# Kernel optimization log

Measured on AMD Instinct MI355X. Metric: run time of the kernel, lower is better.

## Reference

```python
import jax, jax.numpy as jnp
import numpy as np

N_PAPER = 50000
N_AUTHOR = 50000
E = 400000
N_FEAT = 256
N_HID = 256
N_CLASS = 128
TEMP = 1.0  # cfg.temparature


def setup_inputs() -> dict:
    key = jax.random.key(0)
    ks = jax.random.split(key, 40)
    def lin_init(k, shape, fan_in):
        s = 1.0 / np.sqrt(fan_in)
        return jax.random.uniform(k, shape, jnp.float32, -s, s)
    inp = {}
    inp['x_paper'] = jax.random.normal(ks[0], (N_PAPER, N_FEAT), jnp.float32)
    # xavier-uniform embedding for featureless node type 'author'
    xs = np.sqrt(6.0 / (N_AUTHOR + N_FEAT))
    inp['emb_author'] = jax.random.uniform(ks[1], (N_AUTHOR, N_FEAT), jnp.float32, -xs, xs)
    i = 2
    for l, fin in [(0, N_FEAT), (1, N_HID)]:
        for nt in ['paper', 'author']:
            inp[f'l{l}_root_{nt}_W'] = lin_init(ks[i], (fin, N_HID), fin); i += 1
            inp[f'l{l}_root_{nt}_b'] = lin_init(ks[i], (N_HID,), fin); i += 1
        for et in ['writes', 'rev', 'cites']:
            inp[f'l{l}_rel_{et}_W'] = lin_init(ks[i], (fin, N_HID), fin); i += 1
    inp['out_W'] = lin_init(ks[i], (N_HID, N_CLASS), N_HID); i += 1
    inp['out_b'] = lin_init(ks[i], (N_CLASS,), N_HID); i += 1
    inp['writes_src'] = jax.random.randint(ks[i], (E,), 0, N_AUTHOR); i += 1
    inp['writes_dst'] = jax.random.randint(ks[i], (E,), 0, N_PAPER); i += 1
    inp['rev_src'] = jax.random.randint(ks[i], (E,), 0, N_PAPER); i += 1
    inp['rev_dst'] = jax.random.randint(ks[i], (E,), 0, N_AUTHOR); i += 1
    inp['cites_src'] = jax.random.randint(ks[i], (E,), 0, N_PAPER); i += 1
    inp['cites_dst'] = jax.random.randint(ks[i], (E,), 0, N_PAPER); i += 1
    return inp


def _mean_agg(x_src, src, dst, n_dst):
    # sparse adj_t.matmul(x, reduce='mean'): segment-sum of gathered rows / in-degree (0 for isolated)
    msg = jax.ops.segment_sum(x_src[src], dst, num_segments=n_dst)  # [n_dst, d]
    deg = jax.ops.segment_sum(jnp.ones(src.shape[0], x_src.dtype), dst, num_segments=n_dst)
    return jnp.where(deg[:, None] > 0, msg / jnp.maximum(deg, 1.0)[:, None], 0.0)


def reference(x_paper, emb_author,
              l0_root_paper_W, l0_root_paper_b, l0_root_author_W, l0_root_author_b,
              l0_rel_writes_W, l0_rel_rev_W, l0_rel_cites_W,
              l1_root_paper_W, l1_root_paper_b, l1_root_author_W, l1_root_author_b,
              l1_rel_writes_W, l1_rel_rev_W, l1_rel_cites_W,
              out_W, out_b,
              writes_src, writes_dst, rev_src, rev_dst, cites_src, cites_dst):
    nnodes = {'paper': x_paper.shape[0], 'author': emb_author.shape[0]}
    # (src_type, dst_type, src_idx, dst_idx, rel_slot)
    edges = [('author', 'paper', writes_src, writes_dst, 0),
             ('paper', 'author', rev_src, rev_dst, 1),
             ('paper', 'paper', cites_src, cites_dst, 2)]
    layers = [
        {'root': {'paper': (l0_root_paper_W, l0_root_paper_b), 'author': (l0_root_author_W, l0_root_author_b)},
         'rel': [l0_rel_writes_W, l0_rel_rev_W, l0_rel_cites_W]},
        {'root': {'paper': (l1_root_paper_W, l1_root_paper_b), 'author': (l1_root_author_W, l1_root_author_b)},
         'rel': [l1_rel_writes_W, l1_rel_rev_W, l1_rel_cites_W]},
    ]
    xd = {'paper': x_paper, 'author': emb_author}
    xd_ = dict(xd)  # twin path starts from same features
    hs, hs_ = [], []
    for p in layers:
        out = {k: xd[k] @ p['root'][k][0] + p['root'][k][1] for k in xd}
        out_ = {k: xd_[k] @ p['root'][k][0] + p['root'][k][1] for k in xd_}
        for s, d, src, dst, slot in edges:
            W = p['rel'][slot]
            out[d] = out[d] + _mean_agg(xd[s], src, dst, nnodes[d]) @ W
            out_[d] = out_[d] + xd_[d] @ W  # twin path: no propagation, same rel transform
        xd = {k: jax.nn.relu(v) for k, v in out.items()}   # dropout is identity (eval)
        xd_ = {k: jax.nn.relu(v) for k, v in out_.items()}
        hs.append(xd['paper'])
        hs_.append(xd_['paper'])
    # Summarize: per-node dot-product attention over layer representations
    H = jnp.stack(hs)    # [L, N, d]
    H_ = jnp.stack(hs_)  # [L, N, d]
    alpha = jax.nn.softmax(jnp.sum(H * H_, axis=-1) / TEMP, axis=0)  # [L, N]
    h = jnp.sum(alpha[..., None] * H, axis=0)  # [N, d]
    logits = h @ out_W + out_b
    return (logits, alpha)
```

## Files before the change

kernel.cpp:

```cpp
#include <hip/hip_runtime.h>
#include <hip/hip_bf16.h>

#define NFEAT 256

typedef __attribute__((ext_vector_type(8))) short bf16x8;
typedef __attribute__((ext_vector_type(4))) float f32x4;
typedef __attribute__((ext_vector_type(8))) unsigned short us8;

__device__ __forceinline__ void f2hilo(float x, unsigned short& h, unsigned short& l) {
    __hip_bfloat16 hb = __float2bfloat16(x);
    float hf = __bfloat162float(hb);
    __hip_bfloat16 lb = __float2bfloat16(x - hf);
    h = *reinterpret_cast<unsigned short*>(&hb);
    l = *reinterpret_cast<unsigned short*>(&lb);
}

__global__ __launch_bounds__(256) void cvt8_kernel(
    const float* w0, const float* w1, const float* w2, const float* w3,
    const float* w4, const float* w5, const float* w6, const float* w7,
    unsigned short* base)
{
    int wi = blockIdx.y;
    const float* W = (wi==0)?w0:(wi==1)?w1:(wi==2)?w2:(wi==3)?w3:
                     (wi==4)?w4:(wi==5)?w5:(wi==6)?w6:w7;
    int idx = blockIdx.x * 256 + threadIdx.x;
    int k = idx >> 8, c = idx & 255;
    unsigned short h, l;
    f2hilo(W[idx], h, l);
    size_t dst = ((size_t)((c >> 7) * 8 + (k >> 5)) * 128 + (c & 127)) * 32 + (k & 31);
    unsigned short* Th = base + (size_t)wi * 131072;
    Th[dst] = h;
    Th[65536 + dst] = l;
}

__global__ __launch_bounds__(256) void cvtfold_kernel(
    const float* a0, const float* a1, const float* a2,
    const float* b0, const float* b1, const float* b2,
    unsigned short* base)
{
    int wi = blockIdx.y;
    int idx = blockIdx.x * 256 + threadIdx.x;
    float v = wi ? (b0[idx] + b1[idx] + b2[idx]) : (a0[idx] + a1[idx] + a2[idx]);
    int k = idx >> 8, c = idx & 255;
    unsigned short h, l;
    f2hilo(v, h, l);
    size_t dst = ((size_t)((c >> 7) * 8 + (k >> 5)) * 128 + (c & 127)) * 32 + (k & 31);
    unsigned short* Th = base + (size_t)(8 + wi) * 131072;
    Th[dst] = h;
    Th[65536 + dst] = l;
}

__global__ __launch_bounds__(256) void cvtrect_kernel(const float* W, unsigned short* base) {
    int idx = blockIdx.x * 256 + threadIdx.x;
    if (idx >= 256 * 128) return;
    int k = idx >> 7, c = idx & 127;
    unsigned short h, l;
    f2hilo(W[idx], h, l);
    size_t dst = ((size_t)(k >> 5) * 128 + c) * 32 + (k & 31);
    unsigned short* Th = base + (size_t)10 * 131072;
    Th[dst] = h;
    Th[65536 + dst] = l;
}

__global__ __launch_bounds__(256) void deg_int_kernel(const int* __restrict__ dst,
                                                      int* __restrict__ deg, int nE) {
    int e = blockIdx.x * 256 + threadIdx.x;
    if (e < nE) atomicAdd(&deg[dst[e]], 1);
}

__global__ __launch_bounds__(256) void scan_p1(const int* __restrict__ deg, int n,
                                               int* __restrict__ off, int* __restrict__ bsum) {
    __shared__ int tmp[256];
    int tid = threadIdx.x;
    int i = blockIdx.x * 256 + tid;
    tmp[tid] = (i < n) ? deg[i] : 0;
    __syncthreads();
    #pragma unroll
    for (int ofs = 1; ofs < 256; ofs <<= 1) {
        int t = (tid >= ofs) ? tmp[tid - ofs] : 0;
        __syncthreads();
        tmp[tid] += t;
        __syncthreads();
    }
    if (i < n) off[i + 1] = tmp[tid];
    if (tid == 255) bsum[blockIdx.x] = tmp[255];
}

__global__ __launch_bounds__(256) void scan_p2(int* __restrict__ bA, int nA,
                                               int* __restrict__ bB, int nB,
                                               int* __restrict__ bC, int nC) {
    int* bs; int nb;
    if (blockIdx.x == 0) { bs = bA; nb = nA; }
    else if (blockIdx.x == 1) { bs = bB; nb = nB; }
    else { bs = bC; nb = nC; }
// ... 48 lines not shown
        acc.x += v.x; acc.y += v.y; acc.z += v.z; acc.w += v.w;
    }
    int cnt = end - start;
    float inv = (cnt > 0) ? 1.0f / (float)cnt : 0.0f;
    float4 d;
    if (mode_add) {
        d = ((float4*)(D + (size_t)r * NFEAT))[lane];
        d.x += acc.x * inv; d.y += acc.y * inv;
        d.z += acc.z * inv; d.w += acc.w * inv;
    } else {
        d.x = acc.x * inv; d.y = acc.y * inv;
        d.z = acc.z * inv; d.w = acc.w * inv;
    }
    if (do_relu) {
        d.x = fmaxf(d.x, 0.f); d.y = fmaxf(d.y, 0.f);
        d.z = fmaxf(d.z, 0.f); d.w = fmaxf(d.w, 0.f);
    }
    ((float4*)(D + (size_t)r * NFEAT))[lane] = d;
}

__global__ __launch_bounds__(256) void alpha_kernel(const float* __restrict__ s0,
                                                    const float* __restrict__ s1,
                                                    float* __restrict__ alpha, int M) {
    int n = blockIdx.x * 256 + threadIdx.x;
    if (n >= M) return;
    float v0 = s0[n], v1 = s1[n];
    float m = fmaxf(v0, v1);
    float e0 = expf(v0 - m), e1 = expf(v1 - m);
    float inv = 1.0f / (e0 + e1);
    alpha[n]     = e0 * inv;
    alpha[M + n] = e1 * inv;
}


struct Seg3 {
    const float *A0, *A1, *A2;
    const unsigned short *Wh0, *Wl0, *Wh1, *Wl1, *Wh2, *Wl2;
};

__global__ __launch_bounds__(256, 3) void gemm_ms(
    Seg3 sp, int nseg, const float* __restrict__ bias, int do_relu,
    float* __restrict__ C, int M, int N)
{
    __shared__ unsigned short Ah[128 * 32];
    __shared__ unsigned short Al[128 * 32];

    int tid = threadIdx.x;
    int lane = tid & 63;
    int w = tid >> 6;
    int wr = w >> 1, wc = w & 1;
    int row0 = blockIdx.x * 128, cb = blockIdx.y, col0 = cb * 128;
    int fr = lane & 15;
    int fg = lane >> 4;

    int sr = tid & 127;
    int sh = tid >> 7;
    int grow = row0 + sr; if (grow >= M) grow = M - 1;
    int wbase = (((sr >> 4) * 64) + (sh * 2) * 16 + (sr & 15)) * 8;

    f32x4 acc[4][4];
    #pragma unroll
    for (int m = 0; m < 4; ++m)
        #pragma unroll
        for (int n = 0; n < 4; ++n)
            acc[m][n] = (f32x4)(0.f);

    for (int s = 0; s < 3; ++s) {
        if (s >= nseg) break;
        const float* Xrow = ((s == 0) ? sp.A0 : (s == 1) ? sp.A1 : sp.A2) + (size_t)grow * NFEAT;
        const unsigned short* Wh = (s == 0) ? sp.Wh0 : (s == 1) ? sp.Wh1 : sp.Wh2;
        const unsigned short* Wl = (s == 0) ? sp.Wl0 : (s == 1) ? sp.Wl1 : sp.Wl2;

        for (int k0 = 0; k0 < NFEAT; k0 += 32) {
            unsigned short hh[16], ll[16];
            #pragma unroll
            for (int q = 0; q < 4; ++q) {
                float4 v = *(const float4*)(Xrow + k0 + sh * 16 + q * 4);
                f2hilo(v.x, hh[q*4+0], ll[q*4+0]);
                f2hilo(v.y, hh[q*4+1], ll[q*4+1]);
                f2hilo(v.z, hh[q*4+2], ll[q*4+2]);
                f2hilo(v.w, hh[q*4+3], ll[q*4+3]);
            }
            __syncthreads();
            *(us8*)&Ah[wbase]       = *(us8*)&hh[0];
            *(us8*)&Ah[wbase + 128] = *(us8*)&hh[8];
            *(us8*)&Al[wbase]       = *(us8*)&ll[0];
            *(us8*)&Al[wbase + 128] = *(us8*)&ll[8];
            __syncthreads();

            const unsigned short* WhB = Wh + (size_t)(cb * 8 + (k0 >> 5)) * 4096;
            const unsigned short* WlB = Wl + (size_t)(cb * 8 + (k0 >> 5)) * 4096;

            bf16x8 ahf[4], alf[4], bhf[4], blf[4];
            #pragma unroll
            for (int m = 0; m < 4; ++m) {
                int g = ((wr * 4 + m) * 64 + lane) * 8;
                ahf[m] = *(const bf16x8*)&Ah[g];
                alf[m] = *(const bf16x8*)&Al[g];
            }
            #pragma unroll
            for (int n = 0; n < 4; ++n) {
                int o = (wc * 64 + n * 16 + fr) * 32 + fg * 8;
                bhf[n] = *(const bf16x8*)(WhB + o);
                blf[n] = *(const bf16x8*)(WlB + o);
            }
            #pragma unroll
            for (int m = 0; m < 4; ++m)
                #pragma unroll
                for (int n = 0; n < 4; ++n) {
                    acc[m][n] = __builtin_amdgcn_mfma_f32_16x16x32_bf16(ahf[m], bhf[n], acc[m][n], 0, 0, 0);
                    acc[m][n] = __builtin_amdgcn_mfma_f32_16x16x32_bf16(alf[m], bhf[n], acc[m][n], 0, 0, 0);
                    acc[m][n] = __builtin_amdgcn_mfma_f32_16x16x32_bf16(ahf[m], blf[n], acc[m][n], 0, 0, 0);
                }
        }
    }

    #pragma unroll
    for (int n = 0; n < 4; ++n) {
        int c = col0 + wc * 64 + n * 16 + fr;
        float bv = bias ? bias[c] : 0.f;
        #pragma unroll
        for (int m = 0; m < 4; ++m) {
            int rbase = row0 + wr * 64 + m * 16 + fg * 4;
            #pragma unroll
            for (int i = 0; i < 4; ++i) {
                int r = rbase + i;
                if (r < M) {
                    float v = acc[m][n][i] + bv;
                    if (do_relu) v = fmaxf(v, 0.f);
                    C[(size_t)r * N + c] = v;
                }
            }
        }
    }
}

__global__ __launch_bounds__(256, 3) void gemm_rowdot_mfma(
    const float* __restrict__ X,
    const unsigned short* __restrict__ Wh, const unsigned short* __restrict__ Wl,
    const float* __restrict__ bias,
    const float* __restrict__ P, const float* __restrict__ Q,
    float* __restrict__ s0g, float* __restrict__ s1g, int M)
{
    __shared__ unsigned short Ah[128 * 32];
    __shared__ unsigned short Al[128 * 32];
    __shared__ float srow[128];
    __shared__ float s0buf[256];

    int tid = threadIdx.x;
    int lane = tid & 63;
    int w = tid >> 6;
    int wr = w >> 1, wc = w & 1;
    int row0 = blockIdx.x * 128;
    int fr = lane & 15;
    int fg = lane >> 4;

    int sr = tid & 127;
    int sh = tid >> 7;
    int grow = row0 + sr; if (grow >= M) grow = M - 1;
    int wbase = (((sr >> 4) * 64) + (sh * 2) * 16 + (sr & 15)) * 8;

    if (tid < 128) srow[tid] = 0.f;
    float s0part = 0.f;

    const float* Xrow = X + (size_t)grow * NFEAT;
    const float* Qrow = Q + (size_t)grow * NFEAT;

    float rp[4][4];
    #pragma unroll
    for (int m = 0; m < 4; ++m)
        #pragma unroll
        for (int i = 0; i < 4; ++i) rp[m][i] = 0.f;

    for (int ct = 0; ct < 2; ++ct) {
        f32x4 acc[4][4];
        #pragma unroll
        for (int m = 0; m < 4; ++m)
            #pragma unroll
            for (int n = 0; n < 4; ++n)
                acc[m][n] = (f32x4)(0.f);

        for (int k0 = 0; k0 < NFEAT; k0 += 32) {
            unsigned short hh[16], ll[16];
            #pragma unroll
            for (int q = 0; q < 4; ++q) {
                float4 v = *(const float4*)(Xrow + k0 + sh * 16 + q * 4);
                if (ct == 0) {
                    float4 qv = *(const float4*)(Qrow + k0 + sh * 16 + q * 4);
                    s0part += v.x * qv.x + v.y * qv.y + v.z * qv.z + v.w * qv.w;
                }
                f2hilo(v.x, hh[q*4+0], ll[q*4+0]);
                f2hilo(v.y, hh[q*4+1], ll[q*4+1]);
                f2hilo(v.z, hh[q*4+2], ll[q*4+2]);
                f2hilo(v.w, hh[q*4+3], ll[q*4+3]);
            }
            __syncthreads();
            *(us8*)&Ah[wbase]       = *(us8*)&hh[0];
            *(us8*)&Ah[wbase + 128] = *(us8*)&hh[8];
            *(us8*)&Al[wbase]       = *(us8*)&ll[0];
            *(us8*)&Al[wbase + 128] = *(us8*)&ll[8];
            __syncthreads();

            const unsigned short* WhB = Wh + (size_t)(ct * 8 + (k0 >> 5)) * 4096;
            const unsigned short* WlB = Wl + (size_t)(ct * 8 + (k0 >> 5)) * 4096;

            bf16x8 ahf[4], alf[4], bhf[4], blf[4];
            #pragma unroll
            for (int m = 0; m < 4; ++m) {
                int g = ((wr * 4 + m) * 64 + lane) * 8;
                ahf[m] = *(const bf16x8*)&Ah[g];
                alf[m] = *(const bf16x8*)&Al[g];
            }
            #pragma unroll
            for (int n = 0; n < 4; ++n) {
                int o = (wc * 64 + n * 16 + fr) * 32 + fg * 8;
                bhf[n] = *(const bf16x8*)(WhB + o);
                blf[n] = *(const bf16x8*)(WlB + o);
            }
            #pragma unroll
            for (int m = 0; m < 4; ++m)
                #pragma unroll
                for (int n = 0; n < 4; ++n) {
                    acc[m][n] = __builtin_amdgcn_mfma_f32_16x16x32_bf16(ahf[m], bhf[n], acc[m][n], 0, 0, 0);
                    acc[m][n] = __builtin_amdgcn_mfma_f32_16x16x32_bf16(alf[m], bhf[n], acc[m][n], 0, 0, 0);
                    acc[m][n] = __builtin_amdgcn_mfma_f32_16x16x32_bf16(ahf[m], blf[n], acc[m][n], 0, 0, 0);
                }
        }

        int col0 = ct * 128;
        #pragma unroll
        for (int n = 0; n < 4; ++n) {
            int c = col0 + wc * 64 + n * 16 + fr;
            float bv = bias[c];
            #pragma unroll
            for (int m = 0; m < 4; ++m) {
                #pragma unroll
                for (int i = 0; i < 4; ++i) {
                    int r = row0 + wr * 64 + m * 16 + fg * 4 + i;
                    if (r < M) {
                        float v = fmaxf(acc[m][n][i] + bv, 0.f);
                        rp[m][i] += v * P[(size_t)r * NFEAT + c];
                    }
                }
            }
        }
    }

    s0buf[tid] = s0part;

    #pragma unroll
    for (int o = 1; o < 16; o <<= 1) {
        #pragma unroll
        for (int m = 0; m < 4; ++m)
            #pragma unroll
            for (int i = 0; i < 4; ++i)
                rp[m][i] += __shfl_xor(rp[m][i], o);
    }
    if ((lane & 15) == 0) {
        #pragma unroll
        for (int m = 0; m < 4; ++m)
            #pragma unroll
            for (int i = 0; i < 4; ++i)
                atomicAdd(&srow[wr * 64 + m * 16 + fg * 4 + i], rp[m][i]);
    }
    __syncthreads();
    if (tid < 128 && row0 + tid < M) {
        s1g[row0 + tid] = srow[tid];
        s0g[row0 + tid] = s0buf[tid] + s0buf[tid + 128];
    }
}

__global__ __launch_bounds__(256, 3) void gemm_head(
    const float* __restrict__ P1, const float* __restrict__ P2,
    const float* __restrict__ alpha,
    const unsigned short* __restrict__ Wh, const unsigned short* __restrict__ Wl,
    const float* __restrict__ bias,
    float* __restrict__ C, int M, int N)
{
    __shared__ unsigned short Ah[128 * 32];
    __shared__ unsigned short Al[128 * 32];

    int tid = threadIdx.x;
    int lane = tid & 63;
    int w = tid >> 6;
    int wr = w >> 1, wc = w & 1;
    int row0 = blockIdx.x * 128;
    int fr = lane & 15;
    int fg = lane >> 4;

    int sr = tid & 127;
    int sh = tid >> 7;
    int grow = row0 + sr; if (grow >= M) grow = M - 1;
    int wbase = (((sr >> 4) * 64) + (sh * 2) * 16 + (sr & 15)) * 8;

    const float* P1row = P1 + (size_t)grow * NFEAT;
    const float* P2row = P2 + (size_t)grow * NFEAT;
    float a0 = alpha[grow], a1 = alpha[M + grow];

    f32x4 acc[4][4];
    #pragma unroll
    for (int m = 0; m < 4; ++m)
        #pragma unroll
        for (int n = 0; n < 4; ++n)
            acc[m][n] = (f32x4)(0.f);

    for (int k0 = 0; k0 < NFEAT; k0 += 32) {
        unsigned short hh[16], ll[16];
        #pragma unroll
        for (int q = 0; q < 4; ++q) {
            float4 u = *(const float4*)(P1row + k0 + sh * 16 + q * 4);
            float4 v = *(const float4*)(P2row + k0 + sh * 16 + q * 4);
            float4 x = make_float4(a0*u.x + a1*v.x, a0*u.y + a1*v.y,
                                   a0*u.z + a1*v.z, a0*u.w + a1*v.w);
            f2hilo(x.x, hh[q*4+0], ll[q*4+0]);
            f2hilo(x.y, hh[q*4+1], ll[q*4+1]);
            f2hilo(x.z, hh[q*4+2], ll[q*4+2]);
            f2hilo(x.w, hh[q*4+3], ll[q*4+3]);
        }
        __syncthreads();
        *(us8*)&Ah[wbase]       = *(us8*)&hh[0];
        *(us8*)&Ah[wbase + 128] = *(us8*)&hh[8];
        *(us8*)&Al[wbase]       = *(us8*)&ll[0];
        *(us8*)&Al[wbase + 128] = *(us8*)&ll[8];
        __syncthreads();

        const unsigned short* WhB = Wh + (size_t)(k0 >> 5) * 4096;
        const unsigned short* WlB = Wl + (size_t)(k0 >> 5) * 4096;

        bf16x8 ahf[4], alf[4], bhf[4], blf[4];
        #pragma unroll
        for (int m = 0; m < 4; ++m) {
            int g = ((wr * 4 + m) * 64 + lane) * 8;
            ahf[m] = *(const bf16x8*)&Ah[g];
            alf[m] = *(const bf16x8*)&Al[g];
        }
        #pragma unroll
        for (int n = 0; n < 4; ++n) {
            int o = (wc * 64 + n * 16 + fr) * 32 + fg * 8;
            bhf[n] = *(const bf16x8*)(WhB + o);
            blf[n] = *(const bf16x8*)(WlB + o);
        }
        #pragma unroll
        for (int m = 0; m < 4; ++m)
            #pragma unroll
            for (int n = 0; n < 4; ++n) {
                acc[m][n] = __builtin_amdgcn_mfma_f32_16x16x32_bf16(ahf[m], bhf[n], acc[m][n], 0, 0, 0);
                acc[m][n] = __builtin_amdgcn_mfma_f32_16x16x32_bf16(alf[m], bhf[n], acc[m][n], 0, 0, 0);
                acc[m][n] = __builtin_amdgcn_mfma_f32_16x16x32_bf16(ahf[m], blf[n], acc[m][n], 0, 0, 0);
            }
    }

    #pragma unroll
    for (int n = 0; n < 4; ++n) {
        int c = wc * 64 + n * 16 + fr;
        if (c >= N) continue;
        float bv = bias[c];
        #pragma unroll
        for (int m = 0; m < 4; ++m) {
            int rbase = row0 + wr * 64 + m * 16 + fg * 4;
            #pragma unroll
            for (int i = 0; i < 4; ++i) {
                int r = rbase + i;
                if (r < M) C[(size_t)r * N + c] = acc[m][n][i] + bv;
            }
        }
    }
}

extern "C" void kernel_launch(void* const* d_in, const int* in_sizes, int n_in,
                              void* d_out, int out_size, void* d_ws, size_t ws_size,
                              hipStream_t stream)
{
    const float* x_paper    = (const float*)d_in[0];
// ... 44 lines not shown
    int* bsW  = offC + NP + 1;
    int* bsR  = bsW + 256;
    int* bsC  = bsR + 256;
    int* listW = bsC + 256;
    int* listR = listW + nEw;
    int* listC = listR + nEr;

    float* out   = (float*)d_out;
    float* alpha = out + (size_t)NP * NC;

    hipMemsetAsync(degW, 0, (size_t)2 * (NP + NA + NP) * sizeof(int), stream);
    deg_int_kernel<<<(nEw + 255) / 256, 256, 0, stream>>>(w_dst, degW, nEw);
    deg_int_kernel<<<(nEr + 255) / 256, 256, 0, stream>>>(r_dst, degR, nEr);
    deg_int_kernel<<<(nEc + 255) / 256, 256, 0, stream>>>(c_dst, degC, nEc);

    int nbP = (NP + 255) / 256, nbA = (NA + 255) / 256;
    scan_p1<<<nbP, 256, 0, stream>>>(degW, NP, offW, bsW);
    scan_p1<<<nbA, 256, 0, stream>>>(degR, NA, offR, bsR);
    scan_p1<<<nbP, 256, 0, stream>>>(degC, NP, offC, bsC);
    scan_p2<<<3, 256, 0, stream>>>(bsW, nbP, bsR, nbA, bsC, nbP);
    scan_p3<<<nbP, 256, 0, stream>>>(NP, offW, bsW);
    scan_p3<<<nbA, 256, 0, stream>>>(NA, offR, bsR);
    scan_p3<<<nbP, 256, 0, stream>>>(NP, offC, bsC);

    fill_csr_kernel<<<(nEw + 255) / 256, 256, 0, stream>>>(w_src, w_dst, nEw, offW, curW, listW);
    fill_csr_kernel<<<(nEr + 255) / 256, 256, 0, stream>>>(r_src, r_dst, nEr, offR, curR, listR);
    fill_csr_kernel<<<(nEc + 255) / 256, 256, 0, stream>>>(c_src, c_dst, nEc, offC, curC, listC);

    cvt8_kernel<<<dim3(256, 8), 256, 0, stream>>>(W0rp, W0w, W0c, W0ra, W0rev, W1rp, W1w, W1c, Wt);
    cvtfold_kernel<<<dim3(256, 2), 256, 0, stream>>>(W0rp, W0w, W0c, W1rp, W1w, W1c, Wt);
    cvtrect_kernel<<<128, 256, 0, stream>>>(outW, Wt);

    dim3 blk(256);
    dim3 gP((NP + 127) / 128, 2);
    dim3 gA((NA + 127) / 128, 2);
    dim3 g1((NP + 127) / 128);
    int nodeP = (NP + 3) / 4, nodeA = (NA + 3) / 4;

    agg_csr_kernel<<<nodeP, blk, 0, stream>>>(emb_author, offW, listW, Z0, 0, 0, NP);
    agg_csr_kernel<<<nodeP, blk, 0, stream>>>(x_paper,    offC, listC, Z1, 0, 0, NP);
    {
        Seg3 sp = {x_paper, Z0, Z1, WT_HI(0), WT_LO(0), WT_HI(1), WT_LO(1), WT_HI(2), WT_LO(2)};
        gemm_ms<<<gP, blk, 0, stream>>>(sp, 3, b0rp, 1, Z2, NP, NFEAT);
    }
    agg_csr_kernel<<<nodeA, blk, 0, stream>>>(x_paper, offR, listR, Z0, 0, 0, NA);
    {
        Seg3 sp = {emb_author, Z0, nullptr, WT_HI(3), WT_LO(3), WT_HI(4), WT_LO(4), nullptr, nullptr};
        gemm_ms<<<gA, blk, 0, stream>>>(sp, 2, b0ra, 1, Z1, NA, NFEAT);
    }

    agg_csr_kernel<<<nodeP, blk, 0, stream>>>(Z1, offW, listW, Z0, 0, 0, NP);
    {
        Seg3 sp = {Z2, Z0, nullptr, WT_HI(5), WT_LO(5), WT_HI(6), WT_LO(6), nullptr, nullptr};
        gemm_ms<<<gP, blk, 0, stream>>>(sp, 2, b1rp, 0, Z1, NP, NFEAT);
    }
    {
        Seg3 sp = {Z2, nullptr, nullptr, WT_HI(7), WT_LO(7), nullptr, nullptr, nullptr, nullptr};
        gemm_ms<<<gP, blk, 0, stream>>>(sp, 1, nullptr, 0, Z0, NP, NFEAT);
    }
    agg_csr_kernel<<<nodeP, blk, 0, stream>>>(Z0, offC, listC, Z1, 1, 1, NP);

    {
        Seg3 sp = {x_paper, nullptr, nullptr, WT_HI(8), WT_LO(8), nullptr, nullptr, nullptr, nullptr};
        gemm_ms<<<gP, blk, 0, stream>>>(sp, 1, b0rp, 1, Z0, NP, NFEAT);
    }
    gemm_rowdot_mfma<<<g1, blk, 0, stream>>>(Z0, WT_HI(9), WT_LO(9), b1rp, Z1, Z2, s0, s1, NP);

    alpha_kernel<<<(NP + 255) / 256, blk, 0, stream>>>(s0, s1, alpha, NP);
// ... 3 lines not shown
```

Measured before the change: 948.1 us.

## Prefetch next K-tile into registers and stage weights through LDS in GEMMs

The three MFMA GEMM kernels now issue the global loads for the next K-slice (activations and bf16 hi/lo weights) right after the LDS barrier, so they overlap with the current tile's MFMAs. Weights are cooperatively loaded into new shared-memory B tiles instead of being read directly from global memory by each wave. The row-dot kernel flattens its two column passes into one 16-step pipelined loop, and gemm_ms interleaves its two column blocks along grid x so neighbouring blocks share A rows. LDS per block doubles and the occupancy hint drops from 3 to 2 blocks per CU, which may limit latency hiding.

Result: no change. 949.5 us (+0.1%).

```diff
diff --git a/kernel.cpp b/kernel.cpp
--- a/kernel.cpp
+++ b/kernel.cpp
@@ -13,6 +13,25 @@
     __hip_bfloat16 lb = __float2bfloat16(x - hf);
     h = *reinterpret_cast<unsigned short*>(&hb);
     l = *reinterpret_cast<unsigned short*>(&lb);
+}
+
+__device__ __forceinline__ void load_a16(const float* __restrict__ p, float* af) {
+    float4 u0 = ((const float4*)p)[0];
+    float4 u1 = ((const float4*)p)[1];
+    float4 u2 = ((const float4*)p)[2];
+    float4 u3 = ((const float4*)p)[3];
+    af[0]=u0.x; af[1]=u0.y; af[2]=u0.z; af[3]=u0.w;
+    af[4]=u1.x; af[5]=u1.y; af[6]=u1.z; af[7]=u1.w;
+    af[8]=u2.x; af[9]=u2.y; af[10]=u2.z; af[11]=u2.w;
+    af[12]=u3.x; af[13]=u3.y; af[14]=u3.z; af[15]=u3.w;
+}
+
+__device__ __forceinline__ void load_b(const unsigned short* __restrict__ ph,
+                                       const unsigned short* __restrict__ pl, us8* bb) {
+    bb[0] = *(const us8*)ph;
+    bb[1] = *(const us8*)(ph + 8);
+    bb[2] = *(const us8*)pl;
+    bb[3] = *(const us8*)(pl + 8);
 }
 
 __global__ __launch_bounds__(256) void cvt8_kernel(
@@ -174,24 +193,26 @@
     alpha[M + n] = e1 * inv;
 }
 
-
 struct Seg3 {
     const float *A0, *A1, *A2;
     const unsigned short *Wh0, *Wl0, *Wh1, *Wl1, *Wh2, *Wl2;
 };
 
-__global__ __launch_bounds__(256, 3) void gemm_ms(
+__global__ __launch_bounds__(256, 2) void gemm_ms(
     Seg3 sp, int nseg, const float* __restrict__ bias, int do_relu,
     float* __restrict__ C, int M, int N)
 {
     __shared__ unsigned short Ah[128 * 32];
     __shared__ unsigned short Al[128 * 32];
+    __shared__ unsigned short Bh[128 * 32];
+    __shared__ unsigned short Bl[128 * 32];
 
     int tid = threadIdx.x;
     int lane = tid & 63;
     int w = tid >> 6;
     int wr = w >> 1, wc = w & 1;
-    int row0 = blockIdx.x * 128, cb = blockIdx.y, col0 = cb * 128;
+    int rb = blockIdx.x >> 1, cb = blockIdx.x & 1;
+    int row0 = rb * 128, col0 = cb * 128;
     int fr = lane & 15;
     int fg = lane >> 4;
 
@@ -200,6 +221,10 @@
     int grow = row0 + sr; if (grow >= M) grow = M - 1;
     int wbase = (((sr >> 4) * 64) + (sh * 2) * 16 + (sr & 15)) * 8;
 
+    int bc = tid >> 1;
+    int bk = (tid & 1) * 16;
+    int bbase = (((bc >> 4) * 64) + (tid & 1) * 2 * 16 + (bc & 15)) * 8;
+
     f32x4 acc[4][4];
     #pragma unroll
     for (int m = 0; m < 4; ++m)
@@ -207,54 +232,59 @@
         for (int n = 0; n < 4; ++n)
             acc[m][n] = (f32x4)(0.f);
 
-    for (int s = 0; s < 3; ++s) {
-        if (s >= nseg) break;
-        const float* Xrow = ((s == 0) ? sp.A0 : (s == 1) ? sp.A1 : sp.A2) + (size_t)grow * NFEAT;
-        const unsigned short* Wh = (s == 0) ? sp.Wh0 : (s == 1) ? sp.Wh1 : sp.Wh2;
-        const unsigned short* Wl = (s == 0) ? sp.Wl0 : (s == 1) ? sp.Wl1 : sp.Wl2;
-
-        for (int k0 = 0; k0 < NFEAT; k0 += 32) {
-            unsigned short hh[16], ll[16];
-            #pragma unroll
-            for (int q = 0; q < 4; ++q) {
-                float4 v = *(const float4*)(Xrow + k0 + sh * 16 + q * 4);
-                f2hilo(v.x, hh[q*4+0], ll[q*4+0]);
-                f2hilo(v.y, hh[q*4+1], ll[q*4+1]);
-                f2hilo(v.z, hh[q*4+2], ll[q*4+2]);
-                f2hilo(v.w, hh[q*4+3], ll[q*4+3]);
+    int niters = nseg * 8;
+    float af[16];
+    us8 bb[4];
+    load_a16(sp.A0 + (size_t)grow * NFEAT + sh * 16, af);
+    load_b(sp.Wh0 + (size_t)(cb * 8) * 4096 + bc * 32 + bk,
+           sp.Wl0 + (size_t)(cb * 8) * 4096 + bc * 32 + bk, bb);
+
+    for (int it = 0; it < niters; ++it) {
+        unsigned short hh[16], ll[16];
+        #pragma unroll
+        for (int j = 0; j < 16; ++j) f2hilo(af[j], hh[j], ll[j]);
+        __syncthreads();
+        *(us8*)&Ah[wbase]       = *(us8*)&hh[0];
+        *(us8*)&Ah[wbase + 128] = *(us8*)&hh[8];
+        *(us8*)&Al[wbase]       = *(us8*)&ll[0];
+        *(us8*)&Al[wbase + 128] = *(us8*)&ll[8];
+        *(us8*)&Bh[bbase]       = bb[0];
+        *(us8*)&Bh[bbase + 128] = bb[1];
+        *(us8*)&Bl[bbase]       = bb[2];
+        *(us8*)&Bl[bbase + 128] = bb[3];
+        __syncthreads();
+
+        if (it + 1 < niters) {
+            int s = (it + 1) >> 3, kq = (it + 1) & 7;
+            const float* A = (s == 0) ? sp.A0 : (s == 1) ? sp.A1 : sp.A2;
+            const unsigned short* Wh = (s == 0) ? sp.Wh0 : (s == 1) ? sp.Wh1 : sp.Wh2;
+            const unsigned short* Wl = (s == 0) ? sp.Wl0 : (s == 1) ? sp.Wl1 : sp.Wl2;
+            load_a16(A + (size_t)grow * NFEAT + kq * 32 + sh * 16, af);
+            load_b(Wh + (size_t)(cb * 8 + kq) * 4096 + bc * 32 + bk,
+                   Wl + (size_t)(cb * 8 + kq) * 4096 + bc * 32 + bk, bb);
+        }
+
+        bf16x8 ahf[4], alf[4], bhf[4], blf[4];
+        #pragma unroll
+        for (int m = 0; m < 4; ++m) {
+            int g = ((wr * 4 + m) * 64 + lane) * 8;
+            ahf[m] = *(const bf16x8*)&Ah[g];
+            alf[m] = *(const bf16x8*)&Al[g];
+        }
+        #pragma unroll
+        for (int n = 0; n < 4; ++n) {
+            int g = ((wc * 4 + n) * 64 + lane) * 8;
+            bhf[n] = *(const bf16x8*)&Bh[g];
+            blf[n] = *(const bf16x8*)&Bl[g];
+        }
+        #pragma unroll
+        for (int m = 0; m < 4; ++m)
+            #pragma unroll
+            for (int n = 0; n < 4; ++n) {
+                acc[m][n] = __builtin_amdgcn_mfma_f32_16x16x32_bf16(ahf[m], bhf[n], acc[m][n], 0, 0, 0);
+                acc[m][n] = __builtin_amdgcn_mfma_f32_16x16x32_bf16(alf[m], bhf[n], acc[m][n], 0, 0, 0);
+                acc[m][n] = __builtin_amdgcn_mfma_f32_16x16x32_bf16(ahf[m], blf[n], acc[m][n], 0, 0, 0);
             }
-            __syncthreads();
-            *(us8*)&Ah[wbase]       = *(us8*)&hh[0];
-            *(us8*)&Ah[wbase + 128] = *(us8*)&hh[8];
-            *(us8*)&Al[wbase]       = *(us8*)&ll[0];
-            *(us8*)&Al[wbase + 128] = *(us8*)&ll[8];
-            __syncthreads();
-
-            const unsigned short* WhB = Wh + (size_t)(cb * 8 + (k0 >> 5)) * 4096;
-            const unsigned short* WlB = Wl + (size_t)(cb * 8 + (k0 >> 5)) * 4096;
-
-            bf16x8 ahf[4], alf[4], bhf[4], blf[4];
-            #pragma unroll
-            for (int m = 0; m < 4; ++m) {
-                int g = ((wr * 4 + m) * 64 + lane) * 8;
-                ahf[m] = *(const bf16x8*)&Ah[g];
-                alf[m] = *(const bf16x8*)&Al[g];
-            }
-            #pragma unroll
-            for (int n = 0; n < 4; ++n) {
-                int o = (wc * 64 + n * 16 + fr) * 32 + fg * 8;
-                bhf[n] = *(const bf16x8*)(WhB + o);
-                blf[n] = *(const bf16x8*)(WlB + o);
-            }
-            #pragma unroll
-            for (int m = 0; m < 4; ++m)
-                #pragma unroll
-                for (int n = 0; n < 4; ++n) {
-                    acc[m][n] = __builtin_amdgcn_mfma_f32_16x16x32_bf16(ahf[m], bhf[n], acc[m][n], 0, 0, 0);
-                    acc[m][n] = __builtin_amdgcn_mfma_f32_16x16x32_bf16(alf[m], bhf[n], acc[m][n], 0, 0, 0);
-                    acc[m][n] = __builtin_amdgcn_mfma_f32_16x16x32_bf16(ahf[m], blf[n], acc[m][n], 0, 0, 0);
-                }
-        }
     }
 
     #pragma unroll
@@ -277,7 +307,7 @@
     }
 }
 
-__global__ __launch_bounds__(256, 3) void gemm_rowdot_mfma(
+__global__ __launch_bounds__(256, 2) void gemm_rowdot_mfma(
     const float* __restrict__ X,
     const unsigned short* __restrict__ Wh, const unsigned short* __restrict__ Wl,
     const float* __restrict__ bias,
@@ -286,6 +316,8 @@
 {
     __shared__ unsigned short Ah[128 * 32];
     __shared__ unsigned short Al[128 * 32];
+    __shared__ unsigned short Bh[128 * 32];
+    __shared__ unsigned short Bl[128 * 32];
     __shared__ float srow[128];
     __shared__ float s0buf[256];
 
@@ -301,12 +333,15 @@
     int sh = tid >> 7;
     int grow = row0 + sr; if (grow >= M) grow = M - 1;
     int wbase = (((sr >> 4) * 64) + (sh * 2) * 16 + (sr & 15)) * 8;
+    int bc = tid >> 1;
+    int bk = (tid & 1) * 16;
+    int bbase = (((bc >> 4) * 64) + (tid & 1) * 2 * 16 + (bc & 15)) * 8;
 
     if (tid < 128) srow[tid] = 0.f;
     float s0part = 0.f;
 
-    const float* Xrow = X + (size_t)grow * NFEAT;
-    const float* Qrow = Q + (size_t)grow * NFEAT;
+    const float* Xrow = X + (size_t)grow * NFEAT + sh * 16;
+    const float* Qrow = Q + (size_t)grow * NFEAT + sh * 16;
 
     float rp[4][4];
     #pragma unroll
@@ -314,77 +349,91 @@
         #pragma unroll
         for (int i = 0; i < 4; ++i) rp[m][i] = 0.f;
 
-    for (int ct = 0; ct < 2; ++ct) {
-        f32x4 acc[4][4];
+    f32x4 acc[4][4];
+    #pragma unroll
+    for (int m = 0; m < 4; ++m)
+        #pragma unroll
+        for (int n = 0; n < 4; ++n)
+            acc[m][n] = (f32x4)(0.f);
+
+    float af[16], qf[16];
+    us8 bb[4];
+    load_a16(Xrow, af);
+    load_a16(Qrow, qf);
+    load_b(Wh + bc * 32 + bk, Wl + bc * 32 + bk, bb);
+
+    for (int it = 0; it < 16; ++it) {
+        if (it < 8) {
+            #pragma unroll
+            for (int j = 0; j < 16; ++j) s0part += af[j] * qf[j];
+        }
+        unsigned short hh[16], ll[16];
+        #pragma unroll
+        for (int j = 0; j < 16; ++j) f2hilo(af[j], hh[j], ll[j]);
+        __syncthreads();
+        *(us8*)&Ah[wbase]       = *(us8*)&hh[0];
+        *(us8*)&Ah[wbase + 128] = *(us8*)&hh[8];
+        *(us8*)&Al[wbase]       = *(us8*)&ll[0];
+        *(us8*)&Al[wbase + 128] = *(us8*)&ll[8];
+        *(us8*)&Bh[bbase]       = bb[0];
+        *(us8*)&Bh[bbase + 128] = bb[1];
+        *(us8*)&Bl[bbase]       = bb[2];
+        *(us8*)&Bl[bbase + 128] = bb[3];
+        __syncthreads();
+
+        if (it + 1 < 16) {
+            int kq = (it + 1) & 7;
+            load_a16(Xrow + kq * 32, af);
+            if (it + 1 < 8) load_a16(Qrow + kq * 32, qf);
+            load_b(Wh + (size_t)(it + 1) * 4096 + bc * 32 + bk,
+                   Wl + (size_t)(it + 1) * 4096 + bc * 32 + bk, bb);
+        }
+
+        bf16x8 ahf[4], alf[4], bhf[4], blf[4];
+        #pragma unroll
+        for (int m = 0; m < 4; ++m) {
+            int g = ((wr * 4 + m) * 64 + lane) * 8;
+            ahf[m] = *(const bf16x8*)&Ah[g];
+            alf[m] = *(const bf16x8*)&Al[g];
+        }
+        #pragma unroll
+        for (int n = 0; n < 4; ++n) {
+            int g = ((wc * 4 + n) * 64 + lane) * 8;
+            bhf[n] = *(const bf16x8*)&Bh[g];
+            blf[n] = *(const bf16x8*)&Bl[g];
+        }
         #pragma unroll
         for (int m = 0; m < 4; ++m)
             #pragma unroll
-            for (int n = 0; n < 4; ++n)
-                acc[m][n] = (f32x4)(0.f);
-
-        for (int k0 = 0; k0 < NFEAT; k0 += 32) {
-            unsigned short hh[16], ll[16];
-            #pragma unroll
-            for (int q = 0; q < 4; ++q) {
-                float4 v = *(const float4*)(Xrow + k0 + sh * 16 + q * 4);
-                if (ct == 0) {
-                    float4 qv = *(const float4*)(Qrow + k0 + sh * 16 + q * 4);
-                    s0part += v.x * qv.x + v.y * qv.y + v.z * qv.z + v.w * qv.w;
-                }
-                f2hilo(v.x, hh[q*4+0], ll[q*4+0]);
-                f2hilo(v.y, hh[q*4+1], ll[q*4+1]);
-                f2hilo(v.z, hh[q*4+2], ll[q*4+2]);
-                f2hilo(v.w, hh[q*4+3], ll[q*4+3]);
+            for (int n = 0; n < 4; ++n) {
+                acc[m][n] = __builtin_amdgcn_mfma_f32_16x16x32_bf16(ahf[m], bhf[n], acc[m][n], 0, 0, 0);
+                acc[m][n] = __builtin_amdgcn_mfma_f32_16x16x32_bf16(alf[m], bhf[n], acc[m][n], 0, 0, 0);
+                acc[m][n] = __builtin_amdgcn_mfma_f32_16x16x32_bf16(ahf[m], blf[n], acc[m][n], 0, 0, 0);
             }
-            __syncthreads();
-            *(us8*)&Ah[wbase]       = *(us8*)&hh[0];
-            *(us8*)&Ah[wbase + 128] = *(us8*)&hh[8];
-            *(us8*)&Al[wbase]       = *(us8*)&ll[0];
-            *(us8*)&Al[wbase + 128] = *(us8*)&ll[8];
-            __syncthreads();
-
-            const unsigned short* WhB = Wh + (size_t)(ct * 8 + (k0 >> 5)) * 4096;
-            const unsigned short* WlB = Wl + (size_t)(ct * 8 + (k0 >> 5)) * 4096;
-
-            bf16x8 ahf[4], alf[4], bhf[4], blf[4];
-            #pragma unroll
-            for (int m = 0; m < 4; ++m) {
-                int g = ((wr * 4 + m) * 64 + lane) * 8;
-                ahf[m] = *(const bf16x8*)&Ah[g];
-                alf[m] = *(const bf16x8*)&Al[g];
-            }
+
+        if ((it & 7) == 7) {
+            int col0 = (it >> 3) * 128;
             #pragma unroll
             for (int n = 0; n < 4; ++n) {
-                int o = (wc * 64 + n * 16 + fr) * 32 + fg * 8;
-                bhf[n] = *(const bf16x8*)(WhB + o);
-                blf[n] = *(const bf16x8*)(WlB + o);
-            }
-            #pragma unroll
-            for (int m = 0; m < 4; ++m)
+                int c = col0 + wc * 64 + n * 16 + fr;
+                float bv = bias[c];
                 #pragma unroll
-                for (int n = 0; n < 4; ++n) {
-                    acc[m][n] = __builtin_amdgcn_mfma_f32_16x16x32_bf16(ahf[m], bhf[n], acc[m][n], 0, 0, 0);
-                    acc[m][n] = __builtin_amdgcn_mfma_f32_16x16x32_bf16(alf[m], bhf[n], acc[m][n], 0, 0, 0);
-                    acc[m][n] = __builtin_amdgcn_mfma_f32_16x16x32_bf16(ahf[m], blf[n], acc[m][n], 0, 0, 0);
-                }
-        }
-
-        int col0 = ct * 128;
-        #pragma unroll
-        for (int n = 0; n < 4; ++n) {
-            int c = col0 + wc * 64 + n * 16 + fr;
-            float bv = bias[c];
-            #pragma unroll
-            for (int m = 0; m < 4; ++m) {
-                #pragma unroll
-                for (int i = 0; i < 4; ++i) {
-                    int r = row0 + wr * 64 + m * 16 + fg * 4 + i;
-                    if (r < M) {
-                        float v = fmaxf(acc[m][n][i] + bv, 0.f);
-                        rp[m][i] += v * P[(size_t)r * NFEAT + c];
+                for (int m = 0; m < 4; ++m) {
+                    #pragma unroll
+                    for (int i = 0; i < 4; ++i) {
+                        int r = row0 + wr * 64 + m * 16 + fg * 4 + i;
+                        if (r < M) {
+                            float v = fmaxf(acc[m][n][i] + bv, 0.f);
+                            rp[m][i] += v * P[(size_t)r * NFEAT + c];
+                        }
                     }
                 }
             }
+            #pragma unroll
+            for (int m = 0; m < 4; ++m)
+                #pragma unroll
+                for (int n = 0; n < 4; ++n)
+                    acc[m][n] = (f32x4)(0.f);
         }
     }
 
@@ -412,7 +461,7 @@
     }
 }
 
-__global__ __launch_bounds__(256, 3) void gemm_head(
+__global__ __launch_bounds__(256, 2) void gemm_head(
     const float* __restrict__ P1, const float* __restrict__ P2,
     const float* __restrict__ alpha,
     const unsigned short* __restrict__ Wh, const unsigned short* __restrict__ Wl,
@@ -421,6 +470,8 @@
 {
     __shared__ unsigned short Ah[128 * 32];
     __shared__ unsigned short Al[128 * 32];
+    __shared__ unsigned short Bh[128 * 32];
+    __shared__ unsigned short Bl[128 * 32];
 
     int tid = threadIdx.x;
     int lane = tid & 63;
@@ -434,9 +485,12 @@
     int sh = tid >> 7;
     int grow = row0 + sr; if (grow >= M) grow = M - 1;
     int wbase = (((sr >> 4) * 64) + (sh * 2) * 16 + (sr & 15)) * 8;
-
-    const float* P1row = P1 + (size_t)grow * NFEAT;
-    const float* P2row = P2 + (size_t)grow * NFEAT;
+    int bc = tid >> 1;
+    int bk = (tid & 1) * 16;
+    int bbase = (((bc >> 4) * 64) + (tid & 1) * 2 * 16 + (bc & 15)) * 8;
+
+    const float* P1row = P1 + (size_t)grow * NFEAT + sh * 16;
+    const float* P2row = P2 + (size_t)grow * NFEAT + sh * 16;
     float a0 = alpha[grow], a1 = alpha[M + grow];
 
     f32x4 acc[4][4];
@@ -446,28 +500,34 @@
         for (int n = 0; n < 4; ++n)
             acc[m][n] = (f32x4)(0.f);
 
-    for (int k0 = 0; k0 < NFEAT; k0 += 32) {
+    float uf[16], vf[16];
+    us8 bb[4];
+    load_a16(P1row, uf);
+    load_a16(P2row, vf);
+    load_b(Wh + bc * 32 + bk, Wl + bc * 32 + bk, bb);
+
+    for (int it = 0; it < 8; ++it) {
         unsigned short hh[16], ll[16];
         #pragma unroll
-        for (int q = 0; q < 4; ++q) {
-            float4 u = *(const float4*)(P1row + k0 + sh * 16 + q * 4);
-            float4 v = *(const float4*)(P2row + k0 + sh * 16 + q * 4);
-            float4 x = make_float4(a0*u.x + a1*v.x, a0*u.y + a1*v.y,
-                                   a0*u.z + a1*v.z, a0*u.w + a1*v.w);
-            f2hilo(x.x, hh[q*4+0], ll[q*4+0]);
-            f2hilo(x.y, hh[q*4+1], ll[q*4+1]);
-            f2hilo(x.z, hh[q*4+2], ll[q*4+2]);
-            f2hilo(x.w, hh[q*4+3], ll[q*4+3]);
-        }
+        for (int j = 0; j < 16; ++j) f2hilo(a0 * uf[j] + a1 * vf[j], hh[j], ll[j]);
         __syncthreads();
         *(us8*)&Ah[wbase]       = *(us8*)&hh[0];
         *(us8*)&Ah[wbase + 128] = *(us8*)&hh[8];
         *(us8*)&Al[wbase]       = *(us8*)&ll[0];
         *(us8*)&Al[wbase + 128] = *(us8*)&ll[8];
-        __syncthreads();
-
-        const unsigned short* WhB = Wh + (size_t)(k0 >> 5) * 4096;
-        const unsigned short* WlB = Wl + (size_t)(k0 >> 5) * 4096;
+        *(us8*)&Bh[bbase]       = bb[0];
+        *(us8*)&Bh[bbase + 128] = bb[1];
+        *(us8*)&Bl[bbase]       = bb[2];
+        *(us8*)&Bl[bbase + 128] = bb[3];
+        __syncthreads();
+
+        if (it + 1 < 8) {
+            int kq = it + 1;
+            load_a16(P1row + kq * 32, uf);
+            load_a16(P2row + kq * 32, vf);
+            load_b(Wh + (size_t)kq * 4096 + bc * 32 + bk,
+                   Wl + (size_t)kq * 4096 + bc * 32 + bk, bb);
+        }
 
         bf16x8 ahf[4], alf[4], bhf[4], blf[4];
         #pragma unroll
@@ -478,9 +538,9 @@
         }
         #pragma unroll
         for (int n = 0; n < 4; ++n) {
-            int o = (wc * 64 + n * 16 + fr) * 32 + fg * 8;
-            bhf[n] = *(const bf16x8*)(WhB + o);
-            blf[n] = *(const bf16x8*)(WlB + o);
+            int g = ((wc * 4 + n) * 64 + lane) * 8;
+            bhf[n] = *(const bf16x8*)&Bh[g];
+            blf[n] = *(const bf16x8*)&Bl[g];
         }
         #pragma unroll
         for (int m = 0; m < 4; ++m)
@@ -591,8 +651,8 @@
     cvtrect_kernel<<<128, 256, 0, stream>>>(outW, Wt);
 
     dim3 blk(256);
-    dim3 gP((NP + 127) / 128, 2);
-    dim3 gA((NA + 127) / 128, 2);
+    dim3 gP(((NP + 127) / 128) * 2);
+    dim3 gA(((NA + 127) / 128) * 2);
     dim3 g1((NP + 127) / 128);
     int nodeP = (NP + 3) / 4, nodeA = (NA + 3) / 4;
 
```

## Stage weight tiles in LDS instead of direct global fragment loads

Applied to the files above, without the earlier changes.

The pre-converted hi/lo bf16 weights are now stored column-major ([c][k]) instead of pre-tiled per MFMA fragment. All three GEMM kernels load a 128x32 weight tile cooperatively into shared memory alongside the activation tile each k-step, and the MFMA B-fragments are read from LDS. This replaces per-wave global fragment reads, which were duplicated across waves, with one coalesced tile load per block. In exchange, shared memory per block doubles and the occupancy hint drops from 3 to 2 blocks per CU.

New measurement: 875.9 us, median of 2. 7.6% less time.

```diff
diff --git a/kernel.cpp b/kernel.cpp
--- a/kernel.cpp
+++ b/kernel.cpp
@@ -14,6 +14,7 @@
     h = *reinterpret_cast<unsigned short*>(&hb);
     l = *reinterpret_cast<unsigned short*>(&lb);
 }
+
 
 __global__ __launch_bounds__(256) void cvt8_kernel(
     const float* w0, const float* w1, const float* w2, const float* w3,
@@ -27,10 +28,9 @@
     int k = idx >> 8, c = idx & 255;
     unsigned short h, l;
     f2hilo(W[idx], h, l);
-    size_t dst = ((size_t)((c >> 7) * 8 + (k >> 5)) * 128 + (c & 127)) * 32 + (k & 31);
     unsigned short* Th = base + (size_t)wi * 131072;
-    Th[dst] = h;
-    Th[65536 + dst] = l;
+    Th[c * 256 + k] = h;
+    Th[65536 + c * 256 + k] = l;
 }
 
 __global__ __launch_bounds__(256) void cvtfold_kernel(
@@ -44,10 +44,9 @@
     int k = idx >> 8, c = idx & 255;
     unsigned short h, l;
     f2hilo(v, h, l);
-    size_t dst = ((size_t)((c >> 7) * 8 + (k >> 5)) * 128 + (c & 127)) * 32 + (k & 31);
     unsigned short* Th = base + (size_t)(8 + wi) * 131072;
-    Th[dst] = h;
-    Th[65536 + dst] = l;
+    Th[c * 256 + k] = h;
+    Th[65536 + c * 256 + k] = l;
 }
 
 __global__ __launch_bounds__(256) void cvtrect_kernel(const float* W, unsigned short* base) {
@@ -56,10 +55,9 @@
     int k = idx >> 7, c = idx & 127;
     unsigned short h, l;
     f2hilo(W[idx], h, l);
-    size_t dst = ((size_t)(k >> 5) * 128 + c) * 32 + (k & 31);
     unsigned short* Th = base + (size_t)10 * 131072;
-    Th[dst] = h;
-    Th[65536 + dst] = l;
+    Th[c * 256 + k] = h;
+    Th[65536 + c * 256 + k] = l;
 }
 
 __global__ __launch_bounds__(256) void deg_int_kernel(const int* __restrict__ dst,
@@ -174,31 +172,33 @@
     alpha[M + n] = e1 * inv;
 }
 
-
 struct Seg3 {
     const float *A0, *A1, *A2;
     const unsigned short *Wh0, *Wl0, *Wh1, *Wl1, *Wh2, *Wl2;
 };
 
-__global__ __launch_bounds__(256, 3) void gemm_ms(
+__global__ __launch_bounds__(256, 2) void gemm_ms(
     Seg3 sp, int nseg, const float* __restrict__ bias, int do_relu,
     float* __restrict__ C, int M, int N)
 {
     __shared__ unsigned short Ah[128 * 32];
     __shared__ unsigned short Al[128 * 32];
+    __shared__ unsigned short Bh[128 * 32];
+    __shared__ unsigned short Bl[128 * 32];
 
     int tid = threadIdx.x;
     int lane = tid & 63;
     int w = tid >> 6;
     int wr = w >> 1, wc = w & 1;
-    int row0 = blockIdx.x * 128, cb = blockIdx.y, col0 = cb * 128;
+    int row0 = blockIdx.x * 128, col0 = blockIdx.y * 128;
     int fr = lane & 15;
     int fg = lane >> 4;
 
-    int sr = tid & 127;
-    int sh = tid >> 7;
+    int sr = tid >> 1;
+    int sk = (tid & 1) * 16;
     int grow = row0 + sr; if (grow >= M) grow = M - 1;
-    int wbase = (((sr >> 4) * 64) + (sh * 2) * 16 + (sr & 15)) * 8;
+    int gcol = col0 + sr;
+    int wbase = ((sr >> 4) * 64 + (sk >> 3) * 16 + (sr & 15)) * 8;
 
     f32x4 acc[4][4];
     #pragma unroll
@@ -210,28 +210,33 @@
     for (int s = 0; s < 3; ++s) {
         if (s >= nseg) break;
         const float* Xrow = ((s == 0) ? sp.A0 : (s == 1) ? sp.A1 : sp.A2) + (size_t)grow * NFEAT;
-        const unsigned short* Wh = (s == 0) ? sp.Wh0 : (s == 1) ? sp.Wh1 : sp.Wh2;
-        const unsigned short* Wl = (s == 0) ? sp.Wl0 : (s == 1) ? sp.Wl1 : sp.Wl2;
+        const unsigned short* WhR = ((s == 0) ? sp.Wh0 : (s == 1) ? sp.Wh1 : sp.Wh2) + (size_t)gcol * NFEAT;
+        const unsigned short* WlR = ((s == 0) ? sp.Wl0 : (s == 1) ? sp.Wl1 : sp.Wl2) + (size_t)gcol * NFEAT;
 
         for (int k0 = 0; k0 < NFEAT; k0 += 32) {
             unsigned short hh[16], ll[16];
             #pragma unroll
             for (int q = 0; q < 4; ++q) {
-                float4 v = *(const float4*)(Xrow + k0 + sh * 16 + q * 4);
+                float4 v = *(const float4*)(Xrow + k0 + sk + q * 4);
                 f2hilo(v.x, hh[q*4+0], ll[q*4+0]);
                 f2hilo(v.y, hh[q*4+1], ll[q*4+1]);
                 f2hilo(v.z, hh[q*4+2], ll[q*4+2]);
                 f2hilo(v.w, hh[q*4+3], ll[q*4+3]);
             }
+            us8 bh0 = *(const us8*)(WhR + k0 + sk);
+            us8 bh1 = *(const us8*)(WhR + k0 + sk + 8);
+            us8 bl0 = *(const us8*)(WlR + k0 + sk);
+            us8 bl1 = *(const us8*)(WlR + k0 + sk + 8);
             __syncthreads();
             *(us8*)&Ah[wbase]       = *(us8*)&hh[0];
             *(us8*)&Ah[wbase + 128] = *(us8*)&hh[8];
             *(us8*)&Al[wbase]       = *(us8*)&ll[0];
             *(us8*)&Al[wbase + 128] = *(us8*)&ll[8];
+            *(us8*)&Bh[wbase]       = bh0;
+            *(us8*)&Bh[wbase + 128] = bh1;
+            *(us8*)&Bl[wbase]       = bl0;
+            *(us8*)&Bl[wbase + 128] = bl1;
             __syncthreads();
-
-            const unsigned short* WhB = Wh + (size_t)(cb * 8 + (k0 >> 5)) * 4096;
-            const unsigned short* WlB = Wl + (size_t)(cb * 8 + (k0 >> 5)) * 4096;
 
             bf16x8 ahf[4], alf[4], bhf[4], blf[4];
             #pragma unroll
@@ -242,9 +247,9 @@
             }
             #pragma unroll
             for (int n = 0; n < 4; ++n) {
-                int o = (wc * 64 + n * 16 + fr) * 32 + fg * 8;
-                bhf[n] = *(const bf16x8*)(WhB + o);
-                blf[n] = *(const bf16x8*)(WlB + o);
+                int g = ((wc * 4 + n) * 64 + lane) * 8;
+                bhf[n] = *(const bf16x8*)&Bh[g];
+                blf[n] = *(const bf16x8*)&Bl[g];
             }
             #pragma unroll
             for (int m = 0; m < 4; ++m)
@@ -277,7 +282,7 @@
     }
 }
 
-__global__ __launch_bounds__(256, 3) void gemm_rowdot_mfma(
+__global__ __launch_bounds__(256, 2) void gemm_rowdot_mfma(
     const float* __restrict__ X,
     const unsigned short* __restrict__ Wh, const unsigned short* __restrict__ Wl,
     const float* __restrict__ bias,
@@ -286,6 +291,8 @@
 {
     __shared__ unsigned short Ah[128 * 32];
     __shared__ unsigned short Al[128 * 32];
+    __shared__ unsigned short Bh[128 * 32];
+    __shared__ unsigned short Bl[128 * 32];
     __shared__ float srow[128];
     __shared__ float s0buf[256];
 
@@ -297,10 +304,10 @@
     int fr = lane & 15;
     int fg = lane >> 4;
 
-    int sr = tid & 127;
-    int sh = tid >> 7;
+    int sr = tid >> 1;
+    int sk = (tid & 1) * 16;
     int grow = row0 + sr; if (grow >= M) grow = M - 1;
-    int wbase = (((sr >> 4) * 64) + (sh * 2) * 16 + (sr & 15)) * 8;
+    int wbase = ((sr >> 4) * 64 + (sk >> 3) * 16 + (sr & 15)) * 8;
 
     if (tid < 128) srow[tid] = 0.f;
     float s0part = 0.f;
@@ -315,6 +322,10 @@
         for (int i = 0; i < 4; ++i) rp[m][i] = 0.f;
 
     for (int ct = 0; ct < 2; ++ct) {
+        int col0 = ct * 128;
+        const unsigned short* WhR = Wh + (size_t)(col0 + sr) * NFEAT;
+        const unsigned short* WlR = Wl + (size_t)(col0 + sr) * NFEAT;
+
         f32x4 acc[4][4];
         #pragma unroll
         for (int m = 0; m < 4; ++m)
@@ -326,9 +337,9 @@
             unsigned short hh[16], ll[16];
             #pragma unroll
             for (int q = 0; q < 4; ++q) {
-                float4 v = *(const float4*)(Xrow + k0 + sh * 16 + q * 4);
+                float4 v = *(const float4*)(Xrow + k0 + sk + q * 4);
                 if (ct == 0) {
-                    float4 qv = *(const float4*)(Qrow + k0 + sh * 16 + q * 4);
+                    float4 qv = *(const float4*)(Qrow + k0 + sk + q * 4);
                     s0part += v.x * qv.x + v.y * qv.y + v.z * qv.z + v.w * qv.w;
                 }
                 f2hilo(v.x, hh[q*4+0], ll[q*4+0]);
@@ -336,15 +347,20 @@
                 f2hilo(v.z, hh[q*4+2], ll[q*4+2]);
                 f2hilo(v.w, hh[q*4+3], ll[q*4+3]);
             }
+            us8 bh0 = *(const us8*)(WhR + k0 + sk);
+            us8 bh1 = *(const us8*)(WhR + k0 + sk + 8);
+            us8 bl0 = *(const us8*)(WlR + k0 + sk);
+            us8 bl1 = *(const us8*)(WlR + k0 + sk + 8);
             __syncthreads();
             *(us8*)&Ah[wbase]       = *(us8*)&hh[0];
             *(us8*)&Ah[wbase + 128] = *(us8*)&hh[8];
             *(us8*)&Al[wbase]       = *(us8*)&ll[0];
             *(us8*)&Al[wbase + 128] = *(us8*)&ll[8];
+            *(us8*)&Bh[wbase]       = bh0;
+            *(us8*)&Bh[wbase + 128] = bh1;
+            *(us8*)&Bl[wbase]       = bl0;
+            *(us8*)&Bl[wbase + 128] = bl1;
             __syncthreads();
-
-            const unsigned short* WhB = Wh + (size_t)(ct * 8 + (k0 >> 5)) * 4096;
-            const unsigned short* WlB = Wl + (size_t)(ct * 8 + (k0 >> 5)) * 4096;
 
             bf16x8 ahf[4], alf[4], bhf[4], blf[4];
             #pragma unroll
@@ -355,9 +371,9 @@
             }
             #pragma unroll
             for (int n = 0; n < 4; ++n) {
-                int o = (wc * 64 + n * 16 + fr) * 32 + fg * 8;
-                bhf[n] = *(const bf16x8*)(WhB + o);
-                blf[n] = *(const bf16x8*)(WlB + o);
+                int g = ((wc * 4 + n) * 64 + lane) * 8;
+                bhf[n] = *(const bf16x8*)&Bh[g];
+                blf[n] = *(const bf16x8*)&Bl[g];
             }
             #pragma unroll
             for (int m = 0; m < 4; ++m)
@@ -369,7 +385,6 @@
                 }
         }
 
-        int col0 = ct * 128;
         #pragma unroll
         for (int n = 0; n < 4; ++n) {
             int c = col0 + wc * 64 + n * 16 + fr;
@@ -408,11 +423,11 @@
     __syncthreads();
     if (tid < 128 && row0 + tid < M) {
         s1g[row0 + tid] = srow[tid];
-        s0g[row0 + tid] = s0buf[tid] + s0buf[tid + 128];
-    }
-}
-
-__global__ __launch_bounds__(256, 3) void gemm_head(
+        s0g[row0 + tid] = s0buf[tid * 2] + s0buf[tid * 2 + 1];
+    }
+}
+
+__global__ __launch_bounds__(256, 2) void gemm_head(
     const float* __restrict__ P1, const float* __restrict__ P2,
     const float* __restrict__ alpha,
     const unsigned short* __restrict__ Wh, const unsigned short* __restrict__ Wl,
@@ -421,6 +436,8 @@
 {
     __shared__ unsigned short Ah[128 * 32];
     __shared__ unsigned short Al[128 * 32];
+    __shared__ unsigned short Bh[128 * 32];
+    __shared__ unsigned short Bl[128 * 32];
 
     int tid = threadIdx.x;
     int lane = tid & 63;
@@ -430,14 +447,16 @@
     int fr = lane & 15;
     int fg = lane >> 4;
 
-    int sr = tid & 127;
-    int sh = tid >> 7;
+    int sr = tid >> 1;
+    int sk = (tid & 1) * 16;
     int grow = row0 + sr; if (grow >= M) grow = M - 1;
-    int wbase = (((sr >> 4) * 64) + (sh * 2) * 16 + (sr & 15)) * 8;
+    int wbase = ((sr >> 4) * 64 + (sk >> 3) * 16 + (sr & 15)) * 8;
 
     const float* P1row = P1 + (size_t)grow * NFEAT;
     const float* P2row = P2 + (size_t)grow * NFEAT;
     float a0 = alpha[grow], a1 = alpha[M + grow];
+    const unsigned short* WhR = Wh + (size_t)sr * NFEAT;
+    const unsigned short* WlR = Wl + (size_t)sr * NFEAT;
 
     f32x4 acc[4][4];
     #pragma unroll
@@ -450,8 +469,8 @@
         unsigned short hh[16], ll[16];
         #pragma unroll
         for (int q = 0; q < 4; ++q) {
-            float4 u = *(const float4*)(P1row + k0 + sh * 16 + q * 4);
-            float4 v = *(const float4*)(P2row + k0 + sh * 16 + q * 4);
+            float4 u = *(const float4*)(P1row + k0 + sk + q * 4);
+            float4 v = *(const float4*)(P2row + k0 + sk + q * 4);
             float4 x = make_float4(a0*u.x + a1*v.x, a0*u.y + a1*v.y,
                                    a0*u.z + a1*v.z, a0*u.w + a1*v.w);
             f2hilo(x.x, hh[q*4+0], ll[q*4+0]);
@@ -459,15 +478,20 @@
             f2hilo(x.z, hh[q*4+2], ll[q*4+2]);
             f2hilo(x.w, hh[q*4+3], ll[q*4+3]);
         }
+        us8 bh0 = *(const us8*)(WhR + k0 + sk);
+        us8 bh1 = *(const us8*)(WhR + k0 + sk + 8);
+        us8 bl0 = *(const us8*)(WlR + k0 + sk);
+        us8 bl1 = *(const us8*)(WlR + k0 + sk + 8);
         __syncthreads();
         *(us8*)&Ah[wbase]       = *(us8*)&hh[0];
         *(us8*)&Ah[wbase + 128] = *(us8*)&hh[8];
         *(us8*)&Al[wbase]       = *(us8*)&ll[0];
         *(us8*)&Al[wbase + 128] = *(us8*)&ll[8];
+        *(us8*)&Bh[wbase]       = bh0;
+        *(us8*)&Bh[wbase + 128] = bh1;
+        *(us8*)&Bl[wbase]       = bl0;
+        *(us8*)&Bl[wbase + 128] = bl1;
         __syncthreads();
-
-        const unsigned short* WhB = Wh + (size_t)(k0 >> 5) * 4096;
-        const unsigned short* WlB = Wl + (size_t)(k0 >> 5) * 4096;
 
         bf16x8 ahf[4], alf[4], bhf[4], blf[4];
         #pragma unroll
@@ -478,9 +502,9 @@
         }
         #pragma unroll
         for (int n = 0; n < 4; ++n) {
-            int o = (wc * 64 + n * 16 + fr) * 32 + fg * 8;
-            bhf[n] = *(const bf16x8*)(WhB + o);
-            blf[n] = *(const bf16x8*)(WlB + o);
+            int g = ((wc * 4 + n) * 64 + lane) * 8;
+            bhf[n] = *(const bf16x8*)&Bh[g];
+            blf[n] = *(const bf16x8*)&Bl[g];
         }
         #pragma unroll
         for (int m = 0; m < 4; ++m)
```
